# Kernel optimization log

Measured on AMD Instinct MI355X. Metric: run time of the kernel, lower is better.

## Reference

```python
import jax, jax.numpy as jnp
import numpy as np

NEG_SLOPE = 0.01  # torch nn.LeakyReLU default
K = 16

def lrelu(x):
    return jax.nn.leaky_relu(x, NEG_SLOPE)

def _knn_idx(src, dst, batch_src, batch_dst, k):
    # For each dst node, k nearest src nodes (euclidean, within same graph).
    # [Nd, Ns] squared distances; mask cross-graph pairs with +inf.
    d2 = (jnp.sum(dst * dst, axis=1)[:, None]
          + jnp.sum(src * src, axis=1)[None, :]
          - 2.0 * dst @ src.T)
    d2 = jnp.where(batch_dst[:, None] != batch_src[None, :], jnp.inf, d2)
    _, idx = jax.lax.top_k(-d2, k)  # [Nd, k] indices into src
    return idx

def _dynamic_edge_conv(src, dst, batch_src, batch_dst, w, b, k=K):
    # PyG DynamicEdgeConv: edge_index = knn(src, dst); message = nn([x_i, x_j - x_i]); max-aggregate.
    idx = _knn_idx(src, dst, batch_src, batch_dst, k)
    x_j = src[idx]                      # [Nd, k, D] gathered neighbors
    x_i = dst[:, None, :]               # [Nd, 1, D] center (target) features
    e = jnp.concatenate([jnp.broadcast_to(x_i, x_j.shape), x_j - x_i], axis=-1)  # [Nd, k, 2D]
    h = lrelu(e @ w + b)                # edge MLP: Linear(2D, D) + LeakyReLU
    return jnp.max(h, axis=1)           # max aggregation over k neighbors

def _mlp2(x, w1, b1, w2, b2):
    return lrelu(lrelu(x @ w1 + b1) @ w2 + b2)

def setup_inputs() -> dict:
    key = jax.random.key(0)
    ks = jax.random.split(key, 20)
    N_PFC, N_VTX, G, H = 8192, 2048, 32, 32
    def w(k, shp):
        return 0.1 * jax.random.normal(k, shp, jnp.float32)
    z = lambda n: jnp.zeros((n,), jnp.float32)
    return {
        "x_pfc": jax.random.normal(ks[0], (N_PFC, 7), jnp.float32),
        "x_vtx": jax.random.normal(ks[1], (N_VTX, 4), jnp.float32),
        "batch_pfc": jnp.sort(jax.random.randint(ks[2], (N_PFC,), 0, G)),
        "batch_vtx": jnp.sort(jax.random.randint(ks[3], (N_VTX,), 0, G)),
        "pfc_w1": w(ks[4], (7, H)),  "pfc_b1": z(H),
        "pfc_w2": w(ks[5], (H, H)),  "pfc_b2": z(H),
        "vtx_w1": w(ks[6], (4, H)),  "vtx_b1": z(H),
        "vtx_w2": w(ks[7], (H, H)),  "vtx_b2": z(H),
        "conv_w": w(ks[8], (2 * H, H)), "conv_b": z(H),
        "out_w1": w(ks[9], (H, 64)),  "out_b1": z(64),
        "out_w2": w(ks[10], (64, 32)), "out_b2": z(32),
        "out_w3": w(ks[11], (32, 4)),  "out_b3": z(4),
        "out_w4": w(ks[12], (4, 1)),   "out_b4": z(1),
    }

def reference(x_pfc, x_vtx, batch_pfc, batch_vtx,
              pfc_w1, pfc_b1, pfc_w2, pfc_b2,
              vtx_w1, vtx_b1, vtx_w2, vtx_b2,
              conv_w, conv_b,
              out_w1, out_b1, out_w2, out_b2, out_w3, out_b3, out_w4, out_b4):
    x_pfc_enc = _mlp2(x_pfc, pfc_w1, pfc_b1, pfc_w2, pfc_b2)   # [Npfc, 32]
    x_vtx_enc = _mlp2(x_vtx, vtx_w1, vtx_b1, vtx_w2, vtx_b2)   # [Nvtx, 32]
    # conv 1: pfc -> pfc (self knn)
    feats1 = _dynamic_edge_conv(x_pfc_enc, x_pfc_enc, batch_pfc, batch_pfc, conv_w, conv_b)
    # conv 2: vtx -> pfc (bipartite knn), same shared edge-MLP weights
    feats2 = _dynamic_edge_conv(x_vtx_enc, feats1, batch_vtx, batch_pfc, conv_w, conv_b)
    h = lrelu(feats2 @ out_w1 + out_b1)
    h = lrelu(h @ out_w2 + out_b2)
    h = lrelu(h @ out_w3 + out_b3)
    out = lrelu(h @ out_w4 + out_b4)    # [Npfc, 1]
    return (out, batch_pfc)
```

## Files before the change

### kernel.cpp

```cpp
#include <hip/hip_runtime.h>
#include <hip/hip_bf16.h>

#define LRELU(val) ((val) >= 0.0f ? (val) : 0.01f * (val))

__device__ __forceinline__ float dot4(float4 a, float4 b, float acc) {
    return fmaf(a.x, b.x, fmaf(a.y, b.y, fmaf(a.z, b.z, fmaf(a.w, b.w, acc))));
}

__device__ __forceinline__ float wdot4(const float* __restrict__ wbase, int c, int q,
                                       float4 a, float acc) {
    acc = fmaf(a.x, wbase[(4 * q + 0) * 32 + c], acc);
    acc = fmaf(a.y, wbase[(4 * q + 1) * 32 + c], acc);
    acc = fmaf(a.z, wbase[(4 * q + 2) * 32 + c], acc);
    acc = fmaf(a.w, wbase[(4 * q + 3) * 32 + c], acc);
    return acc;
}

__device__ inline int lower_bound_i(const int* __restrict__ a, int n, int v) {
    int lo = 0, hi = n;
    while (lo < hi) {
        int m = (lo + hi) >> 1;
        if (a[m] < v) lo = m + 1; else hi = m;
    }
    return lo;
}

__device__ __forceinline__ unsigned slot_key_T4(
    int s, int lane, int start, int len, int Ns,
    const float4* __restrict__ srcT4, const float* __restrict__ srcn, float ni,
    float4 x0, float4 x1, float4 x2, float4 x3,
    float4 x4, float4 x5, float4 x6, float4 x7)
{
    const int o = lane + 64 * s;
    const bool valid = o < len;
    const int j = valid ? (start + o) : min(start, Ns - 1);
    float dot = 0.0f;
    dot = dot4(srcT4[0 * Ns + j], x0, dot);
    dot = dot4(srcT4[1 * Ns + j], x1, dot);
    dot = dot4(srcT4[2 * Ns + j], x2, dot);
    dot = dot4(srcT4[3 * Ns + j], x3, dot);
    dot = dot4(srcT4[4 * Ns + j], x4, dot);
    dot = dot4(srcT4[5 * Ns + j], x5, dot);
    dot = dot4(srcT4[6 * Ns + j], x6, dot);
    dot = dot4(srcT4[7 * Ns + j], x7, dot);
    const float d2 = (ni + srcn[j]) - 2.0f * dot;
    unsigned u = __float_as_uint(d2);
    u = (d2 < 0.0f) ? ~u : (u | 0x80000000u);
    return valid ? u : 0xFFFFFFFFu;
}

template <int NSL>
__device__ __forceinline__ void select_compact(
    unsigned k0, unsigned k1, unsigned k2, unsigned k3, unsigned k4, unsigned k5,
    unsigned T, int start, int Ns, int* __restrict__ widxW, int lane)
{
    const unsigned long long below = (1ull << lane) - 1ull;
    int m = __popcll(__ballot(k0 < T));
    if (NSL > 1) m += __popcll(__ballot(k1 < T));
    if (NSL > 2) m += __popcll(__ballot(k2 < T));
    if (NSL > 3) m += __popcll(__ballot(k3 < T));
    if (NSL > 4) m += __popcll(__ballot(k4 < T));
    if (NSL > 5) m += __popcll(__ballot(k5 < T));
    const int need = 16 - m;
    const unsigned long long e0 = __ballot(k0 == T);
    const unsigned long long e1 = (NSL > 1) ? __ballot(k1 == T) : 0ull;
    const unsigned long long e2 = (NSL > 2) ? __ballot(k2 == T) : 0ull;
    const unsigned long long e3 = (NSL > 3) ? __ballot(k3 == T) : 0ull;
    const unsigned long long e4 = (NSL > 4) ? __ballot(k4 == T) : 0ull;
    const int eq0 = __popcll(e0), eq1 = eq0 + __popcll(e1), eq2 = eq1 + __popcll(e2),
              eq3 = eq2 + __popcll(e3), eq4 = eq3 + __popcll(e4);
    const bool sel0 = (k0 < T) || ((k0 == T) && (__popcll(e0 & below) < need));
    const bool sel1 = (NSL > 1) && ((k1 < T) || ((k1 == T) && (eq0 + __popcll(e1 & below) < need)));
    const bool sel2 = (NSL > 2) && ((k2 < T) || ((k2 == T) && (eq1 + __popcll(e2 & below) < need)));
    const bool sel3 = (NSL > 3) && ((k3 < T) || ((k3 == T) && (eq2 + __popcll(e3 & below) < need)));
    const bool sel4 = (NSL > 4) && ((k4 < T) || ((k4 == T) && (eq3 + __popcll(e4 & below) < need)));
    const bool sel5 = (NSL > 5) && ((k5 < T) || ((k5 == T) && (eq4 + __popcll(__ballot(k5 == T) & below) < need)));
    const unsigned long long s0 = __ballot(sel0);
    const unsigned long long s1 = __ballot(sel1);
    const unsigned long long s2 = __ballot(sel2);
    const unsigned long long s3 = __ballot(sel3);
    const unsigned long long s4 = __ballot(sel4);
    const unsigned long long s5 = __ballot(sel5);
    const int c0 = __popcll(s0), c1 = c0 + __popcll(s1), c2 = c1 + __popcll(s2),
              c3 = c2 + __popcll(s3), c4 = c3 + __popcll(s4);
    if (lane < 16) widxW[lane] = min(start, Ns - 1);
    __builtin_amdgcn_wave_barrier();
    if (sel0) widxW[__popcll(s0 & below)] = start + lane;
    if (NSL > 1 && sel1) widxW[c0 + __popcll(s1 & below)] = start + lane + 64;
    if (NSL > 2 && sel2) widxW[c1 + __popcll(s2 & below)] = start + lane + 128;
    if (NSL > 3 && sel3) widxW[c2 + __popcll(s3 & below)] = start + lane + 192;
    if (NSL > 4 && sel4) widxW[c3 + __popcll(s4 & below)] = start + lane + 256;
    if (NSL > 5 && sel5) widxW[c4 + __popcll(s5 & below)] = start + lane + 320;
    __builtin_amdgcn_wave_barrier();
}

template <int NSL>
__device__ __forceinline__ void conv_pair(
    float4 ax0, float4 ax1, float4 ax2, float4 ax3,
    float4 ax4, float4 ax5, float4 ax6, float4 ax7,
    float niA, int startA, int lenA,
    float4 bx0, float4 bx1, float4 bx2, float4 bx3,
    float4 bx4, float4 bx5, float4 bx6, float4 bx7,
    float niB, int startB, int lenB,
    const float* __restrict__ srcf, const float4* __restrict__ srcT4,
    const float* __restrict__ srcn, int Ns,
    const float* __restrict__ W, const float* __restrict__ Bc,
    float4 w20, float4 w21, float4 w22, float4 w23,
    float4 w24, float4 w25, float4 w26, float4 w27,
    float4* __restrict__ sNbrA, float4* __restrict__ sNbrB,
    int* __restrict__ widxA, int* __restrict__ widxB,
    int lane, float& vOutA, float& vOutB)
{
    unsigned kA0 = 0xFFFFFFFFu, kA1 = 0xFFFFFFFFu, kA2 = 0xFFFFFFFFu,
             kA3 = 0xFFFFFFFFu, kA4 = 0xFFFFFFFFu, kA5 = 0xFFFFFFFFu;
    unsigned kB0 = 0xFFFFFFFFu, kB1 = 0xFFFFFFFFu, kB2 = 0xFFFFFFFFu,
             kB3 = 0xFFFFFFFFu, kB4 = 0xFFFFFFFFu, kB5 = 0xFFFFFFFFu;
    kA0 = slot_key_T4(0, lane, startA, lenA, Ns, srcT4, srcn, niA, ax0, ax1, ax2, ax3, ax4, ax5, ax6, ax7);
    kB0 = slot_key_T4(0, lane, startB, lenB, Ns, srcT4, srcn, niB, bx0, bx1, bx2, bx3, bx4, bx5, bx6, bx7);
    if (NSL > 1) {
        if (lenA > 64)  kA1 = slot_key_T4(1, lane, startA, lenA, Ns, srcT4, srcn, niA, ax0, ax1, ax2, ax3, ax4, ax5, ax6, ax7);
        if (lenB > 64)  kB1 = slot_key_T4(1, lane, startB, lenB, Ns, srcT4, srcn, niB, bx0, bx1, bx2, bx3, bx4, bx5, bx6, bx7);
    }
    if (NSL > 2) {
        if (lenA > 128) kA2 = slot_key_T4(2, lane, startA, lenA, Ns, srcT4, srcn, niA, ax0, ax1, ax2, ax3, ax4, ax5, ax6, ax7);
        if (lenB > 128) kB2 = slot_key_T4(2, lane, startB, lenB, Ns, srcT4, srcn, niB, bx0, bx1, bx2, bx3, bx4, bx5, bx6, bx7);
    }
    if (NSL > 3) {
        if (lenA > 192) kA3 = slot_key_T4(3, lane, startA, lenA, Ns, srcT4, srcn, niA, ax0, ax1, ax2, ax3, ax4, ax5, ax6, ax7);
        if (lenB > 192) kB3 = slot_key_T4(3, lane, startB, lenB, Ns, srcT4, srcn, niB, bx0, bx1, bx2, bx3, bx4, bx5, bx6, bx7);
    }
    if (NSL > 4) {
        if (lenA > 256) kA4 = slot_key_T4(4, lane, startA, lenA, Ns, srcT4, srcn, niA, ax0, ax1, ax2, ax3, ax4, ax5, ax6, ax7);
        if (lenB > 256) kB4 = slot_key_T4(4, lane, startB, lenB, Ns, srcT4, srcn, niB, bx0, bx1, bx2, bx3, bx4, bx5, bx6, bx7);
    }
    if (NSL > 5) {
        if (lenA > 320) kA5 = slot_key_T4(5, lane, startA, lenA, Ns, srcT4, srcn, niA, ax0, ax1, ax2, ax3, ax4, ax5, ax6, ax7);
        if (lenB > 320) kB5 = slot_key_T4(5, lane, startB, lenB, Ns, srcT4, srcn, niB, bx0, bx1, bx2, bx3, bx4, bx5, bx6, bx7);
    }

    unsigned loA = 0x80000000u, hiA = 0xFFFFFFFFu, loB = 0x80000000u, hiB = 0xFFFFFFFFu;
#pragma unroll 1
    for (int it = 0; it < 31; ++it) {
        const unsigned mA = loA + ((hiA - loA) >> 1);
        const unsigned mB = loB + ((hiB - loB) >> 1);
        int cA = __popcll(__ballot(kA0 <= mA));
        int cB = __popcll(__ballot(kB0 <= mB));
        if (NSL > 1) { cA += __popcll(__ballot(kA1 <= mA)); cB += __popcll(__ballot(kB1 <= mB)); }
        if (NSL > 2) { cA += __popcll(__ballot(kA2 <= mA)); cB += __popcll(__ballot(kB2 <= mB)); }
        if (NSL > 3) { cA += __popcll(__ballot(kA3 <= mA)); cB += __popcll(__ballot(kB3 <= mB)); }
        if (NSL > 4) { cA += __popcll(__ballot(kA4 <= mA)); cB += __popcll(__ballot(kB4 <= mB)); }
        if (NSL > 5) { cA += __popcll(__ballot(kA5 <= mA)); cB += __popcll(__ballot(kB5 <= mB)); }
        if (loA != hiA) { if (cA >= 16) hiA = mA; else loA = mA + 1; }
        if (loB != hiB) { if (cB >= 16) hiB = mB; else loB = mB + 1; }
        if (loA == hiA && loB == hiB) break;
    }

    select_compact<NSL>(kA0, kA1, kA2, kA3, kA4, kA5, loA, startA, Ns, widxA, lane);
    select_compact<NSL>(kB0, kB1, kB2, kB3, kB4, kB5, loB, startB, Ns, widxB, lane);

    const int c = lane & 31;
    const int n0 = lane >> 3, qq = lane & 7;
    const int n1 = n0 + 8;
    int jA0 = widxA[n0]; jA0 = ((unsigned)jA0 < (unsigned)Ns) ? jA0 : 0;
    int jA1 = widxA[n1]; jA1 = ((unsigned)jA1 < (unsigned)Ns) ? jA1 : 0;
    int jB0 = widxB[n0]; jB0 = ((unsigned)jB0 < (unsigned)Ns) ? jB0 : 0;
    int jB1 = widxB[n1]; jB1 = ((unsigned)jB1 < (unsigned)Ns) ? jB1 : 0;
    const float4* S = reinterpret_cast<const float4*>(srcf);
    const float4 rA0 = S[(size_t)jA0 * 8 + qq];
    const float4 rA1 = S[(size_t)jA1 * 8 + qq];
    const float4 rB0 = S[(size_t)jB0 * 8 + qq];
    const float4 rB1 = S[(size_t)jB1 * 8 + qq];

    float baseA = Bc[c];
    baseA = wdot4(W, c, 0, ax0, baseA); baseA = wdot4(W, c, 1, ax1, baseA);
    baseA = wdot4(W, c, 2, ax2, baseA); baseA = wdot4(W, c, 3, ax3, baseA);
    baseA = wdot4(W, c, 4, ax4, baseA); baseA = wdot4(W, c, 5, ax5, baseA);
    baseA = wdot4(W, c, 6, ax6, baseA); baseA = wdot4(W, c, 7, ax7, baseA);
    float dA = 0.0f;
    dA = dot4(ax0, w20, dA); dA = dot4(ax1, w21, dA); dA = dot4(ax2, w22, dA); dA = dot4(ax3, w23, dA);
    dA = dot4(ax4, w24, dA); dA = dot4(ax5, w25, dA); dA = dot4(ax6, w26, dA); dA = dot4(ax7, w27, dA);
    const float cbaseA = baseA - dA;

    float baseB = Bc[c];
    baseB = wdot4(W, c, 0, bx0, baseB); baseB = wdot4(W, c, 1, bx1, baseB);
    baseB = wdot4(W, c, 2, bx2, baseB); baseB = wdot4(W, c, 3, bx3, baseB);
    baseB = wdot4(W, c, 4, bx4, baseB); baseB = wdot4(W, c, 5, bx5, baseB);
    baseB = wdot4(W, c, 6, bx6, baseB); baseB = wdot4(W, c, 7, bx7, baseB);
    float dB = 0.0f;
    dB = dot4(bx0, w20, dB); dB = dot4(bx1, w21, dB); dB = dot4(bx2, w22, dB); dB = dot4(bx3, w23, dB);
    dB = dot4(bx4, w24, dB); dB = dot4(bx5, w25, dB); dB = dot4(bx6, w26, dB); dB = dot4(bx7, w27, dB);
    const float cbaseB = baseB - dB;

    sNbrA[n0 * 8 + qq] = rA0;
    sNbrA[n1 * 8 + qq] = rA1;
    sNbrB[n0 * 8 + qq] = rB0;
    sNbrB[n1 * 8 + qq] = rB1;
    __builtin_amdgcn_wave_barrier();

    const int half = lane >> 5;
    float vmA = -__builtin_huge_valf(), vmB = -__builtin_huge_valf();
#pragma unroll 1
    for (int r = 0; r < 8; ++r) {
        const float4* nA = sNbrA + (2 * r + half) * 8;
        const float4* nB = sNbrB + (2 * r + half) * 8;
        float accA = cbaseA, accB = cbaseB;
        accA = dot4(nA[0], w20, accA); accB = dot4(nB[0], w20, accB);
        accA = dot4(nA[1], w21, accA); accB = dot4(nB[1], w21, accB);
        accA = dot4(nA[2], w22, accA); accB = dot4(nB[2], w22, accB);
        accA = dot4(nA[3], w23, accA); accB = dot4(nB[3], w23, accB);
        accA = dot4(nA[4], w24, accA); accB = dot4(nB[4], w24, accB);
        accA = dot4(nA[5], w25, accA); accB = dot4(nB[5], w25, accB);
        accA = dot4(nA[6], w26, accA); accB = dot4(nB[6], w26, accB);
        accA = dot4(nA[7], w27, accA); accB = dot4(nB[7], w27, accB);
        vmA = fmaxf(vmA, LRELU(accA));
        vmB = fmaxf(vmB, LRELU(accB));
    }
    vmA = fmaxf(vmA, __shfl_xor(vmA, 32));
    vmB = fmaxf(vmB, __shfl_xor(vmB, 32));
    vOutA = vmA;
    vOutB = vmB;
}

__launch_bounds__(256)
__global__ void encode_kernel(const float* __restrict__ x_pfc, const float* __restrict__ x_vtx,
                              const int* __restrict__ bpfc, const int* __restrict__ bvtx,
                              const float* __restrict__ pw1, const float* __restrict__ pb1,
                              const float* __restrict__ pw2, const float* __restrict__ pb2,
                              const float* __restrict__ vw1, const float* __restrict__ vb1,
                              const float* __restrict__ vw2, const float* __restrict__ vb2,
                              float* __restrict__ pfc_enc, float* __restrict__ pfc_norm,
                              float* __restrict__ vtx_enc, float* __restrict__ vtx_norm,
                              float* __restrict__ pfc_encT4, float* __restrict__ vtx_encT4,
                              int* __restrict__ goff_pfc, int* __restrict__ goff_vtx) {
    __shared__ float h1s[8][32];
    const int t = threadIdx.x;
    const int c = t & 31;
    const int nl = t >> 5;

    if (blockIdx.x == 0) {
        if (t < 33) goff_pfc[t] = lower_bound_i(bpfc, 8192, t);
        else if (t >= 64 && t < 97) goff_vtx[t - 64] = lower_bound_i(bvtx, 2048, t - 64);
    }

    const bool is_pfc = (blockIdx.x < 1024);
    const int node = (is_pfc ? blockIdx.x : (blockIdx.x - 1024)) * 8 + nl;
    const int din = is_pfc ? 7 : 4;
    const int Nn = is_pfc ? 8192 : 2048;
    const float* __restrict__ xin = is_pfc ? (x_pfc + node * 7) : (x_vtx + node * 4);
    const float* __restrict__ w1 = is_pfc ? pw1 : vw1;
    const float* __restrict__ b1 = is_pfc ? pb1 : vb1;
    const float* __restrict__ w2 = is_pfc ? pw2 : vw2;
    const float* __restrict__ b2 = is_pfc ? pb2 : vb2;
    float* __restrict__ enc   = is_pfc ? pfc_enc : vtx_enc;
    float* __restrict__ encT4 = is_pfc ? pfc_encT4 : vtx_encT4;
    float* __restrict__ nrm   = is_pfc ? pfc_norm : vtx_norm;

    float h1 = b1[c];
    for (int d = 0; d < din; ++d) h1 = fmaf(xin[d], w1[d * 32 + c], h1);
    h1 = LRELU(h1);
    h1s[nl][c] = h1;
    __syncthreads();

    float h2 = b2[c];
#pragma unroll
    for (int d = 0; d < 32; ++d) h2 = fmaf(h1s[nl][d], w2[d * 32 + c], h2);
    h2 = LRELU(h2);
    enc[node * 32 + c] = h2;
    encT4[((size_t)(c >> 2) * Nn + node) * 4 + (c & 3)] = h2;

    float s = h2 * h2;
#pragma unroll
    for (int m = 16; m >= 1; m >>= 1) s += __shfl_xor(s, m);
    if (c == 0) nrm[node] = s;
}

__launch_bounds__(128)
__global__ void fused_conv_mlp_kernel(
    const float* __restrict__ pfc_enc, const float4* __restrict__ pfc_encT4,
    const float* __restrict__ n_pfc,
    const float* __restrict__ vtx_enc, const float4* __restrict__ vtx_encT4,
    const float* __restrict__ n_vtx,
    const int* __restrict__ bpfc,
    const int* __restrict__ goff_pfc, const int* __restrict__ goff_vtx,
    const float* __restrict__ W, const float* __restrict__ Bc,
    const float* __restrict__ ow1, const float* __restrict__ ob1,
    const float* __restrict__ ow2, const float* __restrict__ ob2,
    const float* __restrict__ ow3, const float* __restrict__ ob3,
    const float* __restrict__ ow4, const float* __restrict__ ob4,
    float* __restrict__ dout, int N)
{
    __shared__ __align__(16) float4 sNbr[2][2][128];
    __shared__ int widx[2][2][16];
    __shared__ __align__(16) float sRow[2][2][32];
    __shared__ float sEx1[2][2][64];

    const int t = threadIdx.x;
    const int lane = t & 63;
    const int w = t >> 6;
    const int b = blockIdx.x;
    const int xcd = b & 7, chunk = b >> 3;
    const int iA = xcd * 1024 + chunk * 4 + w * 2;
    const int iB = iA + 1;
    const int c = lane & 31;

    const float4 w20 = make_float4(W[32 * 32 + c], W[33 * 32 + c], W[34 * 32 + c], W[35 * 32 + c]);
    const float4 w21 = make_float4(W[36 * 32 + c], W[37 * 32 + c], W[38 * 32 + c], W[39 * 32 + c]);
    const float4 w22 = make_float4(W[40 * 32 + c], W[41 * 32 + c], W[42 * 32 + c], W[43 * 32 + c]);
    const float4 w23 = make_float4(W[44 * 32 + c], W[45 * 32 + c], W[46 * 32 + c], W[47 * 32 + c]);
    const float4 w24 = make_float4(W[48 * 32 + c], W[49 * 32 + c], W[50 * 32 + c], W[51 * 32 + c]);
    const float4 w25 = make_float4(W[52 * 32 + c], W[53 * 32 + c], W[54 * 32 + c], W[55 * 32 + c]);
    const float4 w26 = make_float4(W[56 * 32 + c], W[57 * 32 + c], W[58 * 32 + c], W[59 * 32 + c]);
    const float4 w27 = make_float4(W[60 * 32 + c], W[61 * 32 + c], W[62 * 32 + c], W[63 * 32 + c]);

    float4* sNbrA = &sNbr[w][0][0];
    float4* sNbrB = &sNbr[w][1][0];
    int* widxA = &widx[w][0][0];
    int* widxB = &widx[w][1][0];

    const int gA = bpfc[iA], gB = bpfc[iB];

    const float4* xA = reinterpret_cast<const float4*>(pfc_enc + (size_t)iA * 32);
    const float4 a0 = xA[0], a1 = xA[1], a2 = xA[2], a3 = xA[3],
                 a4 = xA[4], a5 = xA[5], a6 = xA[6], a7 = xA[7];
    const float4* xB = reinterpret_cast<const float4*>(pfc_enc + (size_t)iB * 32);
    const float4 b0 = xB[0], b1 = xB[1], b2 = xB[2], b3 = xB[3],
                 b4 = xB[4], b5 = xB[5], b6 = xB[6], b7 = xB[7];
    const float niA = n_pfc[iA], niB = n_pfc[iB];
    const int s1A = goff_pfc[gA], len1A = min(goff_pfc[gA + 1] - s1A, 384);
    const int s1B = goff_pfc[gB], len1B = min(goff_pfc[gB + 1] - s1B, 384);

    float v1A, v1B;
    {
        const int nsl = (max(len1A, len1B) + 63) >> 6;
        if (nsl <= 4)
            conv_pair<4>(a0, a1, a2, a3, a4, a5, a6, a7, niA, s1A, len1A,
                         b0, b1, b2, b3, b4, b5, b6, b7, niB, s1B, len1B,
                         pfc_enc, pfc_encT4, n_pfc, 8192, W, Bc,
                         w20, w21, w22, w23, w24, w25, w26, w27,
                         sNbrA, sNbrB, widxA, widxB, lane, v1A, v1B);
        else
            conv_pair<6>(a0, a1, a2, a3, a4, a5, a6, a7, niA, s1A, len1A,
                         b0, b1, b2, b3, b4, b5, b6, b7, niB, s1B, len1B,
                         pfc_enc, pfc_encT4, n_pfc, 8192, W, Bc,
                         w20, w21, w22, w23, w24, w25, w26, w27,
                         sNbrA, sNbrB, widxA, widxB, lane, v1A, v1B);
    }

    if (lane < 32) { sRow[w][0][lane] = v1A; sRow[w][1][lane] = v1B; }
    float nfA = v1A * v1A, nfB = v1B * v1B;
#pragma unroll
    for (int m = 16; m >= 1; m >>= 1) { nfA += __shfl_xor(nfA, m); nfB += __shfl_xor(nfB, m); }
    __builtin_amdgcn_wave_barrier();

    const float4* fA = reinterpret_cast<const float4*>(&sRow[w][0][0]);
    const float4 ya0 = fA[0], ya1 = fA[1], ya2 = fA[2], ya3 = fA[3],
                 ya4 = fA[4], ya5 = fA[5], ya6 = fA[6], ya7 = fA[7];
    const float4* fB = reinterpret_cast<const float4*>(&sRow[w][1][0]);
    const float4 yb0 = fB[0], yb1 = fB[1], yb2 = fB[2], yb3 = fB[3],
                 yb4 = fB[4], yb5 = fB[5], yb6 = fB[6], yb7 = fB[7];
    const int s2A = goff_vtx[gA], len2A = min(goff_vtx[gA + 1] - s2A, 128);
    const int s2B = goff_vtx[gB], len2B = min(goff_vtx[gB + 1] - s2B, 128);

    float v2A, v2B;
    conv_pair<2>(ya0, ya1, ya2, ya3, ya4, ya5, ya6, ya7, nfA, s2A, len2A,
                 yb0, yb1, yb2, yb3, yb4, yb5, yb6, yb7, nfB, s2B, len2B,
                 vtx_enc, vtx_encT4, n_vtx, 2048, W, Bc,
                 w20, w21, w22, w23, w24, w25, w26, w27,
                 sNbrA, sNbrB, widxA, widxB, lane, v2A, v2B);

    if (lane < 32) { sRow[w][0][lane] = v2A; sRow[w][1][lane] = v2B; }
    __builtin_amdgcn_wave_barrier();

    {
        float h1a = ob1[lane], h1b = h1a;
#pragma unroll
        for (int d = 0; d < 32; ++d) {
            const float wv = ow1[d * 64 + lane];
            h1a = fmaf(sRow[w][0][d], wv, h1a);
            h1b = fmaf(sRow[w][1][d], wv, h1b);
        }
        sEx1[w][0][lane] = LRELU(h1a);
        sEx1[w][1][lane] = LRELU(h1b);
    }
    __builtin_amdgcn_wave_barrier();

    {
        float h2a = ob2[c], h2b = h2a;
#pragma unroll
        for (int d = 0; d < 64; ++d) {
            const float wv = ow2[d * 32 + c];
            h2a = fmaf(sEx1[w][0][d], wv, h2a);
            h2b = fmaf(sEx1[w][1][d], wv, h2b);
        }
        if (lane < 32) { sRow[w][0][lane] = LRELU(h2a); sRow[w][1][lane] = LRELU(h2b); }
    }
    __builtin_amdgcn_wave_barrier();

    {
        float aa0 = ob3[0], aa1 = ob3[1], aa2 = ob3[2], aa3 = ob3[3];
        float bb0 = aa0, bb1 = aa1, bb2 = aa2, bb3 = aa3;
#pragma unroll
        for (int d = 0; d < 32; ++d) {
            const float ea = sRow[w][0][d], eb = sRow[w][1][d];
            const float w0v = ow3[d * 4 + 0], w1v = ow3[d * 4 + 1],
                        w2v = ow3[d * 4 + 2], w3v = ow3[d * 4 + 3];
            aa0 = fmaf(ea, w0v, aa0); bb0 = fmaf(eb, w0v, bb0);
            aa1 = fmaf(ea, w1v, aa1); bb1 = fmaf(eb, w1v, bb1);
            aa2 = fmaf(ea, w2v, aa2); bb2 = fmaf(eb, w2v, bb2);
            aa3 = fmaf(ea, w3v, aa3); bb3 = fmaf(eb, w3v, bb3);
        }
        aa0 = LRELU(aa0); aa1 = LRELU(aa1); aa2 = LRELU(aa2); aa3 = LRELU(aa3);
        bb0 = LRELU(bb0); bb1 = LRELU(bb1); bb2 = LRELU(bb2); bb3 = LRELU(bb3);
        const float q0 = ow4[0], q1 = ow4[1], q2 = ow4[2], q3 = ow4[3], bz = ob4[0];
        float oA = bz, oB = bz;
        oA = fmaf(aa0, q0, oA); oA = fmaf(aa1, q1, oA); oA = fmaf(aa2, q2, oA); oA = fmaf(aa3, q3, oA);
        oB = fmaf(bb0, q0, oB); oB = fmaf(bb1, q1, oB); oB = fmaf(bb2, q2, oB); oB = fmaf(bb3, q3, oB);
        oA = LRELU(oA); oB = LRELU(oB);

        if (lane == 0) { dout[iA] = oA; dout[iB] = oB; }
        if (lane == 1) { dout[N + iA] = (float)gA; dout[N + iB] = (float)gB; }
    }
}

extern "C" void kernel_launch(void* const* d_in, const int* in_sizes, int n_in,
                              void* d_out, int out_size, void* d_ws, size_t ws_size,
                              hipStream_t stream) {
    const float* x_pfc     = (const float*)d_in[0];
    const float* x_vtx     = (const float*)d_in[1];
    const int*   batch_pfc = (const int*)d_in[2];
    const int*   batch_vtx = (const int*)d_in[3];
    const float* pfc_w1 = (const float*)d_in[4];
    const float* pfc_b1 = (const float*)d_in[5];
    const float* pfc_w2 = (const float*)d_in[6];
    const float* pfc_b2 = (const float*)d_in[7];
    const float* vtx_w1 = (const float*)d_in[8];
    const float* vtx_b1 = (const float*)d_in[9];
    const float* vtx_w2 = (const float*)d_in[10];
    const float* vtx_b2 = (const float*)d_in[11];
    const float* conv_w = (const float*)d_in[12];
    const float* conv_b = (const float*)d_in[13];
    const float* out_w1 = (const float*)d_in[14];
    const float* out_b1 = (const float*)d_in[15];
    const float* out_w2 = (const float*)d_in[16];
    const float* out_b2 = (const float*)d_in[17];
    const float* out_w3 = (const float*)d_in[18];
    const float* out_b3 = (const float*)d_in[19];
    const float* out_w4 = (const float*)d_in[20];
    const float* out_b4 = (const float*)d_in[21];

    const int N_PFC = 8192;

    float* ws = (float*)d_ws;
    float* pfc_enc   = ws;
    float* vtx_enc   = ws + 262144;
    float* n_pfc     = ws + 327680;
    float* n_vtx     = ws + 335872;
    int*   goff_pfc  = (int*)(ws + 337920);
    int*   goff_vtx  = (int*)(ws + 337984);
    float* pfc_encT4 = ws + 338048;
    float* vtx_encT4 = ws + 600192;

    encode_kernel<<<1280, 256, 0, stream>>>(x_pfc, x_vtx, batch_pfc, batch_vtx,
                                            pfc_w1, pfc_b1, pfc_w2, pfc_b2,
                                            vtx_w1, vtx_b1, vtx_w2, vtx_b2,
                                            pfc_enc, n_pfc, vtx_enc, n_vtx,
                                            pfc_encT4, vtx_encT4,
                                            goff_pfc, goff_vtx);

    fused_conv_mlp_kernel<<<2048, 128, 0, stream>>>(
        pfc_enc, (const float4*)pfc_encT4, n_pfc,
        vtx_enc, (const float4*)vtx_encT4, n_vtx,
        batch_pfc, goff_pfc, goff_vtx, conv_w, conv_b,
        out_w1, out_b1, out_w2, out_b2, out_w3, out_b3, out_w4, out_b4,
        (float*)d_out, N_PFC);
}
```

Before: 163.6 us.

## Process one query node per wave and use 4-way radix search for kNN threshold

Replaces the paired two-nodes-per-wave conv routine with a single-node version, launching one 64-thread block per PFC node (8192 blocks). Per-node slice count is now chosen from that node's own graph size rather than the max of a pair. The threshold search changes from a 31-step bisection to a quaternary search with three ballots per step, capped at 20 iterations. The aim is less divergence waste and lower register pressure for higher occupancy. The cost is losing the interleaving of two independent nodes that hid latency, plus more ballots per iteration and a possibly inexact threshold if the iteration cap is hit.

```diff
diff --git a/kernel.cpp b/kernel.cpp
--- a/kernel.cpp
+++ b/kernel.cpp
@@ -95,130 +95,92 @@
 }
 
 template <int NSL>
-__device__ __forceinline__ void conv_pair(
-    float4 ax0, float4 ax1, float4 ax2, float4 ax3,
-    float4 ax4, float4 ax5, float4 ax6, float4 ax7,
-    float niA, int startA, int lenA,
-    float4 bx0, float4 bx1, float4 bx2, float4 bx3,
-    float4 bx4, float4 bx5, float4 bx6, float4 bx7,
-    float niB, int startB, int lenB,
+__device__ __forceinline__ void conv_single(
+    float4 x0, float4 x1, float4 x2, float4 x3,
+    float4 x4, float4 x5, float4 x6, float4 x7,
+    float ni, int start, int len,
     const float* __restrict__ srcf, const float4* __restrict__ srcT4,
     const float* __restrict__ srcn, int Ns,
     const float* __restrict__ W, const float* __restrict__ Bc,
     float4 w20, float4 w21, float4 w22, float4 w23,
     float4 w24, float4 w25, float4 w26, float4 w27,
-    float4* __restrict__ sNbrA, float4* __restrict__ sNbrB,
-    int* __restrict__ widxA, int* __restrict__ widxB,
-    int lane, float& vOutA, float& vOutB)
+    float4* __restrict__ sNbr, int* __restrict__ widxW,
+    int lane, float& vOut)
 {
-    unsigned kA0 = 0xFFFFFFFFu, kA1 = 0xFFFFFFFFu, kA2 = 0xFFFFFFFFu,
-             kA3 = 0xFFFFFFFFu, kA4 = 0xFFFFFFFFu, kA5 = 0xFFFFFFFFu;
-    unsigned kB0 = 0xFFFFFFFFu, kB1 = 0xFFFFFFFFu, kB2 = 0xFFFFFFFFu,
-             kB3 = 0xFFFFFFFFu, kB4 = 0xFFFFFFFFu, kB5 = 0xFFFFFFFFu;
-    kA0 = slot_key_T4(0, lane, startA, lenA, Ns, srcT4, srcn, niA, ax0, ax1, ax2, ax3, ax4, ax5, ax6, ax7);
-    kB0 = slot_key_T4(0, lane, startB, lenB, Ns, srcT4, srcn, niB, bx0, bx1, bx2, bx3, bx4, bx5, bx6, bx7);
-    if (NSL > 1) {
-        if (lenA > 64)  kA1 = slot_key_T4(1, lane, startA, lenA, Ns, srcT4, srcn, niA, ax0, ax1, ax2, ax3, ax4, ax5, ax6, ax7);
-        if (lenB > 64)  kB1 = slot_key_T4(1, lane, startB, lenB, Ns, srcT4, srcn, niB, bx0, bx1, bx2, bx3, bx4, bx5, bx6, bx7);
-    }
-    if (NSL > 2) {
-        if (lenA > 128) kA2 = slot_key_T4(2, lane, startA, lenA, Ns, srcT4, srcn, niA, ax0, ax1, ax2, ax3, ax4, ax5, ax6, ax7);
-        if (lenB > 128) kB2 = slot_key_T4(2, lane, startB, lenB, Ns, srcT4, srcn, niB, bx0, bx1, bx2, bx3, bx4, bx5, bx6, bx7);
-    }
-    if (NSL > 3) {
-        if (lenA > 192) kA3 = slot_key_T4(3, lane, startA, lenA, Ns, srcT4, srcn, niA, ax0, ax1, ax2, ax3, ax4, ax5, ax6, ax7);
-        if (lenB > 192) kB3 = slot_key_T4(3, lane, startB, lenB, Ns, srcT4, srcn, niB, bx0, bx1, bx2, bx3, bx4, bx5, bx6, bx7);
-    }
-    if (NSL > 4) {
-        if (lenA > 256) kA4 = slot_key_T4(4, lane, startA, lenA, Ns, srcT4, srcn, niA, ax0, ax1, ax2, ax3, ax4, ax5, ax6, ax7);
-        if (lenB > 256) kB4 = slot_key_T4(4, lane, startB, lenB, Ns, srcT4, srcn, niB, bx0, bx1, bx2, bx3, bx4, bx5, bx6, bx7);
-    }
-    if (NSL > 5) {
-        if (lenA > 320) kA5 = slot_key_T4(5, lane, startA, lenA, Ns, srcT4, srcn, niA, ax0, ax1, ax2, ax3, ax4, ax5, ax6, ax7);
-        if (lenB > 320) kB5 = slot_key_T4(5, lane, startB, lenB, Ns, srcT4, srcn, niB, bx0, bx1, bx2, bx3, bx4, bx5, bx6, bx7);
-    }
-
-    unsigned loA = 0x80000000u, hiA = 0xFFFFFFFFu, loB = 0x80000000u, hiB = 0xFFFFFFFFu;
+    unsigned k0 = 0xFFFFFFFFu, k1 = 0xFFFFFFFFu, k2 = 0xFFFFFFFFu,
+             k3 = 0xFFFFFFFFu, k4 = 0xFFFFFFFFu, k5 = 0xFFFFFFFFu;
+    k0 = slot_key_T4(0, lane, start, len, Ns, srcT4, srcn, ni, x0, x1, x2, x3, x4, x5, x6, x7);
+    if (NSL > 1 && len > 64)  k1 = slot_key_T4(1, lane, start, len, Ns, srcT4, srcn, ni, x0, x1, x2, x3, x4, x5, x6, x7);
+    if (NSL > 2 && len > 128) k2 = slot_key_T4(2, lane, start, len, Ns, srcT4, srcn, ni, x0, x1, x2, x3, x4, x5, x6, x7);
+    if (NSL > 3 && len > 192) k3 = slot_key_T4(3, lane, start, len, Ns, srcT4, srcn, ni, x0, x1, x2, x3, x4, x5, x6, x7);
+    if (NSL > 4 && len > 256) k4 = slot_key_T4(4, lane, start, len, Ns, srcT4, srcn, ni, x0, x1, x2, x3, x4, x5, x6, x7);
+    if (NSL > 5 && len > 320) k5 = slot_key_T4(5, lane, start, len, Ns, srcT4, srcn, ni, x0, x1, x2, x3, x4, x5, x6, x7);
+
+    unsigned lo = 0x80000000u, hi = 0xFFFFFFFFu;
 #pragma unroll 1
-    for (int it = 0; it < 31; ++it) {
-        const unsigned mA = loA + ((hiA - loA) >> 1);
-        const unsigned mB = loB + ((hiB - loB) >> 1);
-        int cA = __popcll(__ballot(kA0 <= mA));
-        int cB = __popcll(__ballot(kB0 <= mB));
-        if (NSL > 1) { cA += __popcll(__ballot(kA1 <= mA)); cB += __popcll(__ballot(kB1 <= mB)); }
-        if (NSL > 2) { cA += __popcll(__ballot(kA2 <= mA)); cB += __popcll(__ballot(kB2 <= mB)); }
-        if (NSL > 3) { cA += __popcll(__ballot(kA3 <= mA)); cB += __popcll(__ballot(kB3 <= mB)); }
-        if (NSL > 4) { cA += __popcll(__ballot(kA4 <= mA)); cB += __popcll(__ballot(kB4 <= mB)); }
-        if (NSL > 5) { cA += __popcll(__ballot(kA5 <= mA)); cB += __popcll(__ballot(kB5 <= mB)); }
-        if (loA != hiA) { if (cA >= 16) hiA = mA; else loA = mA + 1; }
-        if (loB != hiB) { if (cB >= 16) hiB = mB; else loB = mB + 1; }
-        if (loA == hiA && loB == hiB) break;
-    }
-
-    select_compact<NSL>(kA0, kA1, kA2, kA3, kA4, kA5, loA, startA, Ns, widxA, lane);
-    select_compact<NSL>(kB0, kB1, kB2, kB3, kB4, kB5, loB, startB, Ns, widxB, lane);
+    for (int it = 0; it < 20 && lo < hi; ++it) {
+        const unsigned span = hi - lo;
+        const unsigned q  = span >> 2;
+        const unsigned m1 = lo + q;
+        const unsigned m2 = lo + (span >> 1);
+        const unsigned m3 = hi - q;
+        int c1 = __popcll(__ballot(k0 <= m1));
+        int c2 = __popcll(__ballot(k0 <= m2));
+        int c3 = __popcll(__ballot(k0 <= m3));
+        if (NSL > 1) { c1 += __popcll(__ballot(k1 <= m1)); c2 += __popcll(__ballot(k1 <= m2)); c3 += __popcll(__ballot(k1 <= m3)); }
+        if (NSL > 2) { c1 += __popcll(__ballot(k2 <= m1)); c2 += __popcll(__ballot(k2 <= m2)); c3 += __popcll(__ballot(k2 <= m3)); }
+        if (NSL > 3) { c1 += __popcll(__ballot(k3 <= m1)); c2 += __popcll(__ballot(k3 <= m2)); c3 += __popcll(__ballot(k3 <= m3)); }
+        if (NSL > 4) { c1 += __popcll(__ballot(k4 <= m1)); c2 += __popcll(__ballot(k4 <= m2)); c3 += __popcll(__ballot(k4 <= m3)); }
+        if (NSL > 5) { c1 += __popcll(__ballot(k5 <= m1)); c2 += __popcll(__ballot(k5 <= m2)); c3 += __popcll(__ballot(k5 <= m3)); }
+        if (c1 >= 16) hi = m1;
+        else if (c2 >= 16) { lo = m1 + 1; hi = m2; }
+        else if (c3 >= 16) { lo = m2 + 1; hi = m3; }
+        else lo = m3 + 1;
+    }
+
+    select_compact<NSL>(k0, k1, k2, k3, k4, k5, lo, start, Ns, widxW, lane);
 
     const int c = lane & 31;
     const int n0 = lane >> 3, qq = lane & 7;
     const int n1 = n0 + 8;
-    int jA0 = widxA[n0]; jA0 = ((unsigned)jA0 < (unsigned)Ns) ? jA0 : 0;
-    int jA1 = widxA[n1]; jA1 = ((unsigned)jA1 < (unsigned)Ns) ? jA1 : 0;
-    int jB0 = widxB[n0]; jB0 = ((unsigned)jB0 < (unsigned)Ns) ? jB0 : 0;
-    int jB1 = widxB[n1]; jB1 = ((unsigned)jB1 < (unsigned)Ns) ? jB1 : 0;
+    int j0 = widxW[n0]; j0 = ((unsigned)j0 < (unsigned)Ns) ? j0 : 0;
+    int j1 = widxW[n1]; j1 = ((unsigned)j1 < (unsigned)Ns) ? j1 : 0;
     const float4* S = reinterpret_cast<const float4*>(srcf);
-    const float4 rA0 = S[(size_t)jA0 * 8 + qq];
-    const float4 rA1 = S[(size_t)jA1 * 8 + qq];
-    const float4 rB0 = S[(size_t)jB0 * 8 + qq];
-    const float4 rB1 = S[(size_t)jB1 * 8 + qq];
-
-    float baseA = Bc[c];
-    baseA = wdot4(W, c, 0, ax0, baseA); baseA = wdot4(W, c, 1, ax1, baseA);
-    baseA = wdot4(W, c, 2, ax2, baseA); baseA = wdot4(W, c, 3, ax3, baseA);
-    baseA = wdot4(W, c, 4, ax4, baseA); baseA = wdot4(W, c, 5, ax5, baseA);
-    baseA = wdot4(W, c, 6, ax6, baseA); baseA = wdot4(W, c, 7, ax7, baseA);
-    float dA = 0.0f;
-    dA = dot4(ax0, w20, dA); dA = dot4(ax1, w21, dA); dA = dot4(ax2, w22, dA); dA = dot4(ax3, w23, dA);
-    dA = dot4(ax4, w24, dA); dA = dot4(ax5, w25, dA); dA = dot4(ax6, w26, dA); dA = dot4(ax7, w27, dA);
-    const float cbaseA = baseA - dA;
-
-    float baseB = Bc[c];
-    baseB = wdot4(W, c, 0, bx0, baseB); baseB = wdot4(W, c, 1, bx1, baseB);
-    baseB = wdot4(W, c, 2, bx2, baseB); baseB = wdot4(W, c, 3, bx3, baseB);
-    baseB = wdot4(W, c, 4, bx4, baseB); baseB = wdot4(W, c, 5, bx5, baseB);
-    baseB = wdot4(W, c, 6, bx6, baseB); baseB = wdot4(W, c, 7, bx7, baseB);
-    float dB = 0.0f;
-    dB = dot4(bx0, w20, dB); dB = dot4(bx1, w21, dB); dB = dot4(bx2, w22, dB); dB = dot4(bx3, w23, dB);
-    dB = dot4(bx4, w24, dB); dB = dot4(bx5, w25, dB); dB = dot4(bx6, w26, dB); dB = dot4(bx7, w27, dB);
-    const float cbaseB = baseB - dB;
-
-    sNbrA[n0 * 8 + qq] = rA0;
-    sNbrA[n1 * 8 + qq] = rA1;
-    sNbrB[n0 * 8 + qq] = rB0;
-    sNbrB[n1 * 8 + qq] = rB1;
+    const float4 r0 = S[(size_t)j0 * 8 + qq];
+    const float4 r1 = S[(size_t)j1 * 8 + qq];
+
+    float base = Bc[c];
+    base = wdot4(W, c, 0, x0, base); base = wdot4(W, c, 1, x1, base);
+    base = wdot4(W, c, 2, x2, base); base = wdot4(W, c, 3, x3, base);
+    base = wdot4(W, c, 4, x4, base); base = wdot4(W, c, 5, x5, base);
+    base = wdot4(W, c, 6, x6, base); base = wdot4(W, c, 7, x7, base);
+    float dd = 0.0f;
+    dd = dot4(x0, w20, dd); dd = dot4(x1, w21, dd); dd = dot4(x2, w22, dd); dd = dot4(x3, w23, dd);
+    dd = dot4(x4, w24, dd); dd = dot4(x5, w25, dd); dd = dot4(x6, w26, dd); dd = dot4(x7, w27, dd);
+    const float cbase = base - dd;
+
+    sNbr[n0 * 8 + qq] = r0;
+    sNbr[n1 * 8 + qq] = r1;
     __builtin_amdgcn_wave_barrier();
 
     const int half = lane >> 5;
-    float vmA = -__builtin_huge_valf(), vmB = -__builtin_huge_valf();
+    float vm = -__builtin_huge_valf();
 #pragma unroll 1
     for (int r = 0; r < 8; ++r) {
-        const float4* nA = sNbrA + (2 * r + half) * 8;
-        const float4* nB = sNbrB + (2 * r + half) * 8;
-        float accA = cbaseA, accB = cbaseB;
-        accA = dot4(nA[0], w20, accA); accB = dot4(nB[0], w20, accB);
-        accA = dot4(nA[1], w21, accA); accB = dot4(nB[1], w21, accB);
-        accA = dot4(nA[2], w22, accA); accB = dot4(nB[2], w22, accB);
-        accA = dot4(nA[3], w23, accA); accB = dot4(nB[3], w23, accB);
-        accA = dot4(nA[4], w24, accA); accB = dot4(nB[4], w24, accB);
-        accA = dot4(nA[5], w25, accA); accB = dot4(nB[5], w25, accB);
-        accA = dot4(nA[6], w26, accA); accB = dot4(nB[6], w26, accB);
-        accA = dot4(nA[7], w27, accA); accB = dot4(nB[7], w27, accB);
-        vmA = fmaxf(vmA, LRELU(accA));
-        vmB = fmaxf(vmB, LRELU(accB));
-    }
-    vmA = fmaxf(vmA, __shfl_xor(vmA, 32));
-    vmB = fmaxf(vmB, __shfl_xor(vmB, 32));
-    vOutA = vmA;
-    vOutB = vmB;
+        const float4* nb = sNbr + (2 * r + half) * 8;
+        float acc = cbase;
+        acc = dot4(nb[0], w20, acc);
+        acc = dot4(nb[1], w21, acc);
+        acc = dot4(nb[2], w22, acc);
+        acc = dot4(nb[3], w23, acc);
+        acc = dot4(nb[4], w24, acc);
+        acc = dot4(nb[5], w25, acc);
+        acc = dot4(nb[6], w26, acc);
+        acc = dot4(nb[7], w27, acc);
+        vm = fmaxf(vm, LRELU(acc));
+    }
+    vm = fmaxf(vm, __shfl_xor(vm, 32));
+    vOut = vm;
 }
 
 __launch_bounds__(256)
@@ -274,7 +236,7 @@
     if (c == 0) nrm[node] = s;
 }
 
-__launch_bounds__(128)
+__launch_bounds__(64, 4)
 __global__ void fused_conv_mlp_kernel(
     const float* __restrict__ pfc_enc, const float4* __restrict__ pfc_encT4,
     const float* __restrict__ n_pfc,
@@ -289,18 +251,15 @@
     const float* __restrict__ ow4, const float* __restrict__ ob4,
     float* __restrict__ dout, int N)
 {
-    __shared__ __align__(16) float4 sNbr[2][2][128];
-    __shared__ int widx[2][2][16];
-    __shared__ __align__(16) float sRow[2][2][32];
-    __shared__ float sEx1[2][2][64];
-
-    const int t = threadIdx.x;
-    const int lane = t & 63;
-    const int w = t >> 6;
+    __shared__ __align__(16) float4 sNbr[128];
+    __shared__ int widx[16];
+    __shared__ __align__(16) float sRow[32];
+    __shared__ float sEx1[64];
+
+    const int lane = threadIdx.x & 63;
     const int b = blockIdx.x;
     const int xcd = b & 7, chunk = b >> 3;
-    const int iA = xcd * 1024 + chunk * 4 + w * 2;
-    const int iB = iA + 1;
+    const int i = xcd * 1024 + chunk;
     const int c = lane & 31;
 
     const float4 w20 = make_float4(W[32 * 32 + c], W[33 * 32 + c], W[34 * 32 + c], W[35 * 32 + c]);
@@ -312,113 +271,80 @@
     const float4 w26 = make_float4(W[56 * 32 + c], W[57 * 32 + c], W[58 * 32 + c], W[59 * 32 + c]);
     const float4 w27 = make_float4(W[60 * 32 + c], W[61 * 32 + c], W[62 * 32 + c], W[63 * 32 + c]);
 
-    float4* sNbrA = &sNbr[w][0][0];
-    float4* sNbrB = &sNbr[w][1][0];
-    int* widxA = &widx[w][0][0];
-    int* widxB = &widx[w][1][0];
-
-    const int gA = bpfc[iA], gB = bpfc[iB];
-
-    const float4* xA = reinterpret_cast<const float4*>(pfc_enc + (size_t)iA * 32);
-    const float4 a0 = xA[0], a1 = xA[1], a2 = xA[2], a3 = xA[3],
-                 a4 = xA[4], a5 = xA[5], a6 = xA[6], a7 = xA[7];
-    const float4* xB = reinterpret_cast<const float4*>(pfc_enc + (size_t)iB * 32);
-    const float4 b0 = xB[0], b1 = xB[1], b2 = xB[2], b3 = xB[3],
-                 b4 = xB[4], b5 = xB[5], b6 = xB[6], b7 = xB[7];
-    const float niA = n_pfc[iA], niB = n_pfc[iB];
-    const int s1A = goff_pfc[gA], len1A = min(goff_pfc[gA + 1] - s1A, 384);
-    const int s1B = goff_pfc[gB], len1B = min(goff_pfc[gB + 1] - s1B, 384);
-
-    float v1A, v1B;
+    const int g = bpfc[i];
+
+    const float4* x = reinterpret_cast<const float4*>(pfc_enc + (size_t)i * 32);
+    const float4 a0 = x[0], a1 = x[1], a2 = x[2], a3 = x[3],
+                 a4 = x[4], a5 = x[5], a6 = x[6], a7 = x[7];
+    const float ni = n_pfc[i];
+    const int s1 = goff_pfc[g], len1 = min(goff_pfc[g + 1] - s1, 384);
+
+    float v1;
+    if (((len1 + 63) >> 6) <= 4)
+        conv_single<4>(a0, a1, a2, a3, a4, a5, a6, a7, ni, s1, len1,
+                       pfc_enc, pfc_encT4, n_pfc, 8192, W, Bc,
+                       w20, w21, w22, w23, w24, w25, w26, w27,
+                       sNbr, widx, lane, v1);
+    else
+        conv_single<6>(a0, a1, a2, a3, a4, a5, a6, a7, ni, s1, len1,
+                       pfc_enc, pfc_encT4, n_pfc, 8192, W, Bc,
+                       w20, w21, w22, w23, w24, w25, w26, w27,
+                       sNbr, widx, lane, v1);
+
+    if (lane < 32) sRow[lane] = v1;
+    float nf = v1 * v1;
+#pragma unroll
+    for (int m = 16; m >= 1; m >>= 1) nf += __shfl_xor(nf, m);
+    __builtin_amdgcn_wave_barrier();
+
+    const float4* f = reinterpret_cast<const float4*>(&sRow[0]);
+    const float4 y0 = f[0], y1 = f[1], y2 = f[2], y3 = f[3],
+                 y4 = f[4], y5 = f[5], y6 = f[6], y7 = f[7];
+    const int s2 = goff_vtx[g], len2 = min(goff_vtx[g + 1] - s2, 128);
+
+    float v2;
+    conv_single<2>(y0, y1, y2, y3, y4, y5, y6, y7, nf, s2, len2,
+                   vtx_enc, vtx_encT4, n_vtx, 2048, W, Bc,
+                   w20, w21, w22, w23, w24, w25, w26, w27,
+                   sNbr, widx, lane, v2);
+
+    if (lane < 32) sRow[lane] = v2;
+    __builtin_amdgcn_wave_barrier();
+
     {
-        const int nsl = (max(len1A, len1B) + 63) >> 6;
-        if (nsl <= 4)
-            conv_pair<4>(a0, a1, a2, a3, a4, a5, a6, a7, niA, s1A, len1A,
-                         b0, b1, b2, b3, b4, b5, b6, b7, niB, s1B, len1B,
-                         pfc_enc, pfc_encT4, n_pfc, 8192, W, Bc,
-                         w20, w21, w22, w23, w24, w25, w26, w27,
-                         sNbrA, sNbrB, widxA, widxB, lane, v1A, v1B);
-        else
-            conv_pair<6>(a0, a1, a2, a3, a4, a5, a6, a7, niA, s1A, len1A,
-                         b0, b1, b2, b3, b4, b5, b6, b7, niB, s1B, len1B,
-                         pfc_enc, pfc_encT4, n_pfc, 8192, W, Bc,
-                         w20, w21, w22, w23, w24, w25, w26, w27,
-                         sNbrA, sNbrB, widxA, widxB, lane, v1A, v1B);
-    }
-
-    if (lane < 32) { sRow[w][0][lane] = v1A; sRow[w][1][lane] = v1B; }
-    float nfA = v1A * v1A, nfB = v1B * v1B;
-#pragma unroll
-    for (int m = 16; m >= 1; m >>= 1) { nfA += __shfl_xor(nfA, m); nfB += __shfl_xor(nfB, m); }
-    __builtin_amdgcn_wave_barrier();
-
-    const float4* fA = reinterpret_cast<const float4*>(&sRow[w][0][0]);
-    const float4 ya0 = fA[0], ya1 = fA[1], ya2 = fA[2], ya3 = fA[3],
-                 ya4 = fA[4], ya5 = fA[5], ya6 = fA[6], ya7 = fA[7];
-    const float4* fB = reinterpret_cast<const float4*>(&sRow[w][1][0]);
-    const float4 yb0 = fB[0], yb1 = fB[1], yb2 = fB[2], yb3 = fB[3],
-                 yb4 = fB[4], yb5 = fB[5], yb6 = fB[6], yb7 = fB[7];
-    const int s2A = goff_vtx[gA], len2A = min(goff_vtx[gA + 1] - s2A, 128);
-    const int s2B = goff_vtx[gB], len2B = min(goff_vtx[gB + 1] - s2B, 128);
-
-    float v2A, v2B;
-    conv_pair<2>(ya0, ya1, ya2, ya3, ya4, ya5, ya6, ya7, nfA, s2A, len2A,
-                 yb0, yb1, yb2, yb3, yb4, yb5, yb6, yb7, nfB, s2B, len2B,
-                 vtx_enc, vtx_encT4, n_vtx, 2048, W, Bc,
-                 w20, w21, w22, w23, w24, w25, w26, w27,
-                 sNbrA, sNbrB, widxA, widxB, lane, v2A, v2B);
-
-    if (lane < 32) { sRow[w][0][lane] = v2A; sRow[w][1][lane] = v2B; }
+        float h1 = ob1[lane];
+#pragma unroll
+        for (int d = 0; d < 32; ++d) h1 = fmaf(sRow[d], ow1[d * 64 + lane], h1);
+        sEx1[lane] = LRELU(h1);
+    }
     __builtin_amdgcn_wave_barrier();
 
     {
-        float h1a = ob1[lane], h1b = h1a;
+        float h2 = ob2[c];
+#pragma unroll
+        for (int d = 0; d < 64; ++d) h2 = fmaf(sEx1[d], ow2[d * 32 + c], h2);
+        if (lane < 32) sRow[lane] = LRELU(h2);
+    }
+    __builtin_amdgcn_wave_barrier();
+
+    {
+        float a0_ = ob3[0], a1_ = ob3[1], a2_ = ob3[2], a3_ = ob3[3];
 #pragma unroll
         for (int d = 0; d < 32; ++d) {
-            const float wv = ow1[d * 64 + lane];
-            h1a = fmaf(sRow[w][0][d], wv, h1a);
-            h1b = fmaf(sRow[w][1][d], wv, h1b);
+            const float e = sRow[d];
+            a0_ = fmaf(e, ow3[d * 4 + 0], a0_);
+            a1_ = fmaf(e, ow3[d * 4 + 1], a1_);
+            a2_ = fmaf(e, ow3[d * 4 + 2], a2_);
+            a3_ = fmaf(e, ow3[d * 4 + 3], a3_);
         }
-        sEx1[w][0][lane] = LRELU(h1a);
-        sEx1[w][1][lane] = LRELU(h1b);
-    }
-    __builtin_amdgcn_wave_barrier();
-
-    {
-        float h2a = ob2[c], h2b = h2a;
-#pragma unroll
-        for (int d = 0; d < 64; ++d) {
-            const float wv = ow2[d * 32 + c];
-            h2a = fmaf(sEx1[w][0][d], wv, h2a);
-            h2b = fmaf(sEx1[w][1][d], wv, h2b);
-        }
-        if (lane < 32) { sRow[w][0][lane] = LRELU(h2a); sRow[w][1][lane] = LRELU(h2b); }
-    }
-    __builtin_amdgcn_wave_barrier();
-
-    {
-        float aa0 = ob3[0], aa1 = ob3[1], aa2 = ob3[2], aa3 = ob3[3];
-        float bb0 = aa0, bb1 = aa1, bb2 = aa2, bb3 = aa3;
-#pragma unroll
-        for (int d = 0; d < 32; ++d) {
-            const float ea = sRow[w][0][d], eb = sRow[w][1][d];
-            const float w0v = ow3[d * 4 + 0], w1v = ow3[d * 4 + 1],
-                        w2v = ow3[d * 4 + 2], w3v = ow3[d * 4 + 3];
-            aa0 = fmaf(ea, w0v, aa0); bb0 = fmaf(eb, w0v, bb0);
-            aa1 = fmaf(ea, w1v, aa1); bb1 = fmaf(eb, w1v, bb1);
-            aa2 = fmaf(ea, w2v, aa2); bb2 = fmaf(eb, w2v, bb2);
-            aa3 = fmaf(ea, w3v, aa3); bb3 = fmaf(eb, w3v, bb3);
-        }
-        aa0 = LRELU(aa0); aa1 = LRELU(aa1); aa2 = LRELU(aa2); aa3 = LRELU(aa3);
-        bb0 = LRELU(bb0); bb1 = LRELU(bb1); bb2 = LRELU(bb2); bb3 = LRELU(bb3);
-        const float q0 = ow4[0], q1 = ow4[1], q2 = ow4[2], q3 = ow4[3], bz = ob4[0];
-        float oA = bz, oB = bz;
-        oA = fmaf(aa0, q0, oA); oA = fmaf(aa1, q1, oA); oA = fmaf(aa2, q2, oA); oA = fmaf(aa3, q3, oA);
-        oB = fmaf(bb0, q0, oB); oB = fmaf(bb1, q1, oB); oB = fmaf(bb2, q2, oB); oB = fmaf(bb3, q3, oB);
-        oA = LRELU(oA); oB = LRELU(oB);
-
-        if (lane == 0) { dout[iA] = oA; dout[iB] = oB; }
-        if (lane == 1) { dout[N + iA] = (float)gA; dout[N + iB] = (float)gB; }
+        a0_ = LRELU(a0_); a1_ = LRELU(a1_); a2_ = LRELU(a2_); a3_ = LRELU(a3_);
+        float o = ob4[0];
+        o = fmaf(a0_, ow4[0], o); o = fmaf(a1_, ow4[1], o);
+        o = fmaf(a2_, ow4[2], o); o = fmaf(a3_, ow4[3], o);
+        o = LRELU(o);
+
+        if (lane == 0) dout[i] = o;
+        if (lane == 1) dout[N + i] = (float)g;
     }
 }
 
@@ -467,7 +393,7 @@
                                             pfc_encT4, vtx_encT4,
                                             goff_pfc, goff_vtx);
 
-    fused_conv_mlp_kernel<<<2048, 128, 0, stream>>>(
+    fused_conv_mlp_kernel<<<8192, 64, 0, stream>>>(
         pfc_enc, (const float4*)pfc_encT4, n_pfc,
         vtx_enc, (const float4*)vtx_encT4, n_vtx,
         batch_pfc, goff_pfc, goff_vtx, conv_w, conv_b,
```

Measured after the change: 206.4 us. 1.26x slower.
